# Kernel tuning notes

Hardware: AMD Instinct MI355X
Metric: run time of the kernel (lower is better)

Reference implementation:

```python
import jax, jax.numpy as jnp
import numpy as np

N_NODES = 50000
IN_CH, HID_CH, OUT_CH = 128, 128, 64
N_EDGES = 800000


def setup_inputs() -> dict:
    key = jax.random.key(0)
    k = jax.random.split(key, 6)
    x = jax.random.normal(k[0], (N_NODES, IN_CH), dtype=jnp.float32)
    edge_index = jax.random.randint(k[1], (2, N_EDGES), 0, N_NODES, dtype=jnp.int64)
    # Glorot-ish init for weights
    W1 = jax.random.normal(k[2], (IN_CH, HID_CH), dtype=jnp.float32) * (1.0 / np.sqrt(IN_CH))
    b1 = jnp.zeros((HID_CH,), dtype=jnp.float32)
    W2 = jax.random.normal(k[3], (HID_CH, OUT_CH), dtype=jnp.float32) * (1.0 / np.sqrt(HID_CH))
    b2 = jnp.zeros((OUT_CH,), dtype=jnp.float32)
    return {"x": x, "edge_index": edge_index, "W1": W1, "b1": b1, "W2": W2, "b2": b2}


def _gcn_conv(x, src, dst, W, b, n_nodes):
    """PyG GCNConv: linear, add self-loops, symmetric deg^-1/2 normalization, scatter-add."""
    h = x @ W  # [N, F_out]
    loop = jnp.arange(n_nodes, dtype=src.dtype)
    s = jnp.concatenate([src, loop])  # [E+N]
    d = jnp.concatenate([dst, loop])
    # in-degree on target nodes (including self-loops), edge weight = 1
    deg = jnp.zeros((n_nodes,), dtype=h.dtype).at[d].add(1.0)
    dinv = jnp.where(deg > 0, jax.lax.rsqrt(deg), 0.0)
    norm = dinv[s] * dinv[d]  # [E+N]
    msg = h[s] * norm[:, None]  # [E+N, F_out]
    out = jax.ops.segment_sum(msg, d, num_segments=n_nodes)
    return out + b


def reference(x, edge_index, W1, b1, W2, b2):
    src, dst = edge_index[0], edge_index[1]
    h = _gcn_conv(x, src, dst, W1, b1, N_NODES)
    h = jax.nn.relu(h)
    # dropout in eval mode -> identity
    out = _gcn_conv(h, src, dst, W2, b2, N_NODES)
    return out
```

## Files before the change

kernel.cpp:

```cpp
#include <hip/hip_runtime.h>

typedef __attribute__((ext_vector_type(8))) short bf16x8;
typedef __attribute__((ext_vector_type(4))) float f32x4;

constexpr int NN = 50000;
constexpr int NE = 800000;
constexpr int C1 = 128;
constexpr int C2 = 64;
constexpr int NBK = 196;
constexpr int EPB = 2048;
constexpr int NBLK = (NE + EPB - 1) / EPB;
constexpr int MT = NN / 16;
constexpr int MMB = 250;
constexpr int MMWAVES = MMB * 4;
constexpr int CAP = 8192;

__device__ __forceinline__ unsigned short f2bf(float f) {
    unsigned int u = __float_as_uint(f);
    u += 0x7FFFu + ((u >> 16) & 1u);
    return (unsigned short)(u >> 16);
}
__device__ __forceinline__ float2 bf2f(unsigned int u) {
    return make_float2(__uint_as_float(u << 16), __uint_as_float(u & 0xFFFF0000u));
}
__device__ __forceinline__ bf16x8 pack8(float4 a, float4 b) {
    bf16x8 r;
    r[0] = (short)f2bf(a.x); r[1] = (short)f2bf(a.y);
    r[2] = (short)f2bf(a.z); r[3] = (short)f2bf(a.w);
    r[4] = (short)f2bf(b.x); r[5] = (short)f2bf(b.y);
    r[6] = (short)f2bf(b.z); r[7] = (short)f2bf(b.w);
    return r;
}

__global__ __launch_bounds__(256) void bin_kernel(const int* __restrict__ src,
                                                  const int* __restrict__ dst,
                                                  unsigned int* __restrict__ ebuf,
                                                  int* __restrict__ localOff) {
    __shared__ int lhist[NBK];
    __shared__ int ls[256];
    __shared__ int lcur[NBK];
    __shared__ unsigned int lbuf[EPB];
    const int t = threadIdx.x;
    const int base = blockIdx.x * EPB;
    if (t < NBK) lhist[t] = 0;
    __syncthreads();
    int b[8]; unsigned int p[8];
    #pragma unroll
    for (int i = 0; i < 8; i++) {
        int e = base + i * 256 + t;
        if (e < NE) {
            int s = src[e], d = dst[e];
            b[i] = d >> 8;
            p[i] = ((unsigned int)(d & 255) << 16) | (unsigned int)s;
            atomicAdd(&lhist[b[i]], 1);
        } else b[i] = -1;
    }
    __syncthreads();
    int v = (t < NBK) ? lhist[t] : 0;
    ls[t] = v;
    __syncthreads();
    #pragma unroll
    for (int d = 1; d < 256; d <<= 1) {
        int u = (t >= d) ? ls[t - d] : 0;
        __syncthreads();
        ls[t] += u;
        __syncthreads();
    }
    if (t < NBK) {
        lcur[t] = ls[t] - v;
        localOff[blockIdx.x * 200 + t] = ls[t] - v;
    }
    if (t == NBK - 1) localOff[blockIdx.x * 200 + NBK] = ls[t];
    __syncthreads();
    #pragma unroll
    for (int i = 0; i < 8; i++) {
        if (b[i] >= 0) {
            int lp = atomicAdd(&lcur[b[i]], 1);
            lbuf[lp] = p[i];
        }
    }
    __syncthreads();
    #pragma unroll
    for (int i = 0; i < 8; i++)
        ebuf[base + i * 256 + t] = lbuf[i * 256 + t];
}

__global__ __launch_bounds__(256) void place_kernel(const unsigned int* __restrict__ ebuf,
                                                    const int* __restrict__ localOff,
                                                    unsigned short* __restrict__ esrc,
                                                    int* __restrict__ cnt,
                                                    int* __restrict__ off,
                                                    float* __restrict__ dinv) {
    __shared__ unsigned int lbuf[CAP];
    __shared__ int lhist[256];
    __shared__ int ls[256];
    __shared__ int lcur[256];
    __shared__ int red[256];
    const int t = threadIdx.x;
    const int bkt = blockIdx.x;
    const int node0 = bkt << 8;
    const int nnodes = min(256, NN - node0);

    const int j0 = 2 * t, j1 = 2 * t + 1;
    int s0 = 0, l0 = 0, s1 = 0, l1 = 0;
    if (j0 < NBLK) { s0 = localOff[j0 * 200 + bkt]; l0 = localOff[j0 * 200 + bkt + 1] - s0; }
    if (j1 < NBLK) { s1 = localOff[j1 * 200 + bkt]; l1 = localOff[j1 * 200 + bkt + 1] - s1; }

    red[t] = s0 + s1;
    ls[t] = l0 + l1;
    lhist[t] = 0;
    __syncthreads();
    #pragma unroll
    for (int d = 1; d < 256; d <<= 1) {
        int u = (t >= d) ? ls[t - d] : 0;
        int r = (t + d < 256) ? red[t + d] : 0;
        __syncthreads();
        ls[t] += u;
        red[t] += r;
        __syncthreads();
    }
    const int segBase = red[0];
    const int total = ls[255];
    const int base0 = ls[t] - (l0 + l1);
    const int base1 = base0 + l0;
    const bool fits = (total <= CAP);

    if (fits) {
        const unsigned int* q0 = ebuf + j0 * EPB + s0;
        for (int k = 0; k < l0; k++) lbuf[base0 + k] = q0[k];
        const unsigned int* q1 = ebuf + j1 * EPB + s1;
        for (int k = 0; k < l1; k++) lbuf[base1 + k] = q1[k];
        __syncthreads();
        for (int k = t; k < total; k += 256) atomicAdd(&lhist[lbuf[k] >> 16], 1);
    } else {
        const unsigned int* q0 = ebuf + j0 * EPB + s0;
        for (int k = 0; k < l0; k++) atomicAdd(&lhist[q0[k] >> 16], 1);
        const unsigned int* q1 = ebuf + j1 * EPB + s1;
        for (int k = 0; k < l1; k++) atomicAdd(&lhist[q1[k] >> 16], 1);
    }
    __syncthreads();
    int v = lhist[t];
    ls[t] = v;
    __syncthreads();
    #pragma unroll
    for (int d = 1; d < 256; d <<= 1) {
        int u = (t >= d) ? ls[t - d] : 0;
        __syncthreads();
        ls[t] += u;
        __syncthreads();
    }
    int ex = ls[t] - v;
    lcur[t] = ex;
    if (t < nnodes) {
        cnt[node0 + t] = v;
        off[node0 + t] = segBase + ex;
        dinv[node0 + t] = rsqrtf((float)v + 1.0f);
    }
    __syncthreads();
    if (fits) {
        for (int k = t; k < total; k += 256) {
            unsigned int pp = lbuf[k];
            int lp = atomicAdd(&lcur[pp >> 16], 1);
            esrc[segBase + lp] = (unsigned short)(pp & 0xFFFFu);
        }
    } else {
        const unsigned int* q0 = ebuf + j0 * EPB + s0;
        for (int k = 0; k < l0; k++) {
            unsigned int pp = q0[k];
            int lp = atomicAdd(&lcur[pp >> 16], 1);
            esrc[segBase + lp] = (unsigned short)(pp & 0xFFFFu);
        }
        const unsigned int* q1 = ebuf + j1 * EPB + s1;
        for (int k = 0; k < l1; k++) {
            unsigned int pp = q1[k];
            int lp = atomicAdd(&lcur[pp >> 16], 1);
            esrc[segBase + lp] = (unsigned short)(pp & 0xFFFFu);
        }
    }
}

__global__ __launch_bounds__(256, 2) void mm1_kernel(const float* __restrict__ x,
                                                     const float* __restrict__ W,
                                                     const float* __restrict__ dinv,
                                                     unsigned short* __restrict__ g1s) {
    __shared__ unsigned short wl[4][8][64][8];
    const int t = threadIdx.x;
    for (int i = 0; i < 64; i++) {
        int idx = i * 256 + t;
        int k = idx >> 7, n = idx & 127;
        wl[k >> 5][n >> 4][((k >> 3) & 3) * 16 + (n & 15)][k & 7] = f2bf(W[idx]);
    }
    __syncthreads();
    const int lane = t & 63, lm = lane & 15, quad = lane >> 4;

    bf16x8 bfr[4][8];
    #pragma unroll
    for (int s = 0; s < 4; s++)
        #pragma unroll
        for (int nt = 0; nt < 8; nt++)
            bfr[s][nt] = *(const bf16x8*)&wl[s][nt][lane][0];

    int wg = blockIdx.x * 4 + (t >> 6);
    for (int tile = wg; tile < MT; tile += MMWAVES) {
        int row0 = tile << 4;
        const float* xr = x + (size_t)(row0 + lm) * 128 + quad * 8;
        bf16x8 af[4];
        #pragma unroll
        for (int s = 0; s < 4; s++) {
            float4 p = *(const float4*)(xr + s * 32);
            float4 q = *(const float4*)(xr + s * 32 + 4);
            af[s] = pack8(p, q);
        }
        f32x4 acc[8];
        #pragma unroll
        for (int nt = 0; nt < 8; nt++) acc[nt] = (f32x4){0.f, 0.f, 0.f, 0.f};
        #pragma unroll
        for (int s = 0; s < 4; s++)
            #pragma unroll
            for (int nt = 0; nt < 8; nt++)
                acc[nt] = __builtin_amdgcn_mfma_f32_16x16x32_bf16(af[s], bfr[s][nt],
                                                                  acc[nt], 0, 0, 0);
        float4 dv = *(const float4*)(dinv + row0 + quad * 4);
        float dvv[4] = {dv.x, dv.y, dv.z, dv.w};
        #pragma unroll
        for (int nt = 0; nt < 8; nt++)
            #pragma unroll
            for (int r = 0; r < 4; r++)
                g1s[(size_t)(nt >> 1) * (NN * 32) + (size_t)(row0 + quad * 4 + r) * 32 +
                    (nt & 1) * 16 + lm] = f2bf(acc[nt][r] * dvv[r]);
    }
}

__global__ __launch_bounds__(256, 2) void mm2_kernel(const unsigned short* __restrict__ x2,
                                                     const float* __restrict__ W,
                                                     const float* __restrict__ dinv,
                                                     unsigned short* __restrict__ g2s) {
    __shared__ unsigned short wl[4][4][64][8];
    const int t = threadIdx.x;
    for (int i = 0; i < 32; i++) {
        int idx = i * 256 + t;
        int k = idx >> 6, n = idx & 63;
        wl[k >> 5][n >> 4][((k >> 3) & 3) * 16 + (n & 15)][k & 7] = f2bf(W[idx]);
    }
    __syncthreads();
    const int lane = t & 63, lm = lane & 15, quad = lane >> 4;

    bf16x8 bfr[4][4];
    #pragma unroll
    for (int s = 0; s < 4; s++)
        #pragma unroll
        for (int nt = 0; nt < 4; nt++)
            bfr[s][nt] = *(const bf16x8*)&wl[s][nt][lane][0];

    int wg = blockIdx.x * 4 + (t >> 6);
    for (int tile = wg; tile < MT; tile += MMWAVES) {
        int row0 = tile << 4;
        const bf16x8* xr = (const bf16x8*)(x2 + (size_t)(row0 + lm) * 128 + quad * 8);
        bf16x8 af[4];
        #pragma unroll
        for (int s = 0; s < 4; s++) af[s] = xr[s * 4];
        f32x4 acc[4];
        #pragma unroll
        for (int nt = 0; nt < 4; nt++) acc[nt] = (f32x4){0.f, 0.f, 0.f, 0.f};
        #pragma unroll
        for (int s = 0; s < 4; s++)
            #pragma unroll
            for (int nt = 0; nt < 4; nt++)
                acc[nt] = __builtin_amdgcn_mfma_f32_16x16x32_bf16(af[s], bfr[s][nt],
                                                                  acc[nt], 0, 0, 0);
        float4 dv = *(const float4*)(dinv + row0 + quad * 4);
        float dvv[4] = {dv.x, dv.y, dv.z, dv.w};
        #pragma unroll
        for (int nt = 0; nt < 4; nt++)
            #pragma unroll
            for (int r = 0; r < 4; r++)
                g2s[(size_t)(nt >> 1) * (NN * 32) + (size_t)(row0 + quad * 4 + r) * 32 +
                    (nt & 1) * 16 + lm] = f2bf(acc[nt][r] * dvv[r]);
    }
}

__global__ __launch_bounds__(256) void gp1_kernel(const unsigned int* __restrict__ Gp,
                                                  const unsigned short* __restrict__ esrc,
                                                  const int* __restrict__ off,
                                                  const int* __restrict__ cnt,
                                                  const float* __restrict__ dinv,
                                                  const float* __restrict__ b1,
                                                  unsigned int* __restrict__ x2,
                                                  int pass) {
    const int n = blockIdx.x * 16 + (threadIdx.x >> 4);
    const int p = threadIdx.x & 15;
    float2 a0 = bf2f(Gp[(size_t)n * 16 + p]);
    float2 a1 = make_float2(0.f, 0.f);
    int s0 = off[n], c = cnt[n];
    int i = 0;
    for (; i + 1 < c; i += 2) {
        int sA = esrc[s0 + i];
        int sB = esrc[s0 + i + 1];
        float2 fA = bf2f(Gp[(size_t)sA * 16 + p]);
        float2 fB = bf2f(Gp[(size_t)sB * 16 + p]);
        a0.x += fA.x; a0.y += fA.y;
        a1.x += fB.x; a1.y += fB.y;
    }
    if (i < c) {
        float2 fA = bf2f(Gp[(size_t)esrc[s0 + i] * 16 + p]);
        a0.x += fA.x; a0.y += fA.y;
    }
    a0.x += a1.x; a0.y += a1.y;
    float sc = dinv[n];
    float2 bb = ((const float2*)b1)[pass * 16 + p];
    float lo = fmaxf(sc * a0.x + bb.x, 0.f);
    float hi = fmaxf(sc * a0.y + bb.y, 0.f);
    x2[(size_t)n * 64 + pass * 16 + p] = ((unsigned int)f2bf(hi) << 16) | f2bf(lo);
}

__global__ __launch_bounds__(256) void gp2_kernel(const unsigned int* __restrict__ Gp,
                                                  const unsigned short* __restrict__ esrc,
                                                  const int* __restrict__ off,
                                                  const int* __restrict__ cnt,
                                                  const float* __restrict__ dinv,
                                                  const float* __restrict__ b2,
                                                  float2* __restrict__ out,
                                                  int pass) {
    const int n = blockIdx.x * 16 + (threadIdx.x >> 4);
    const int p = threadIdx.x & 15;
    float2 a0 = bf2f(Gp[(size_t)n * 16 + p]);
    float2 a1 = make_float2(0.f, 0.f);
    int s0 = off[n], c = cnt[n];
    int i = 0;
    for (; i + 1 < c; i += 2) {
        int sA = esrc[s0 + i];
        int sB = esrc[s0 + i + 1];
        float2 fA = bf2f(Gp[(size_t)sA * 16 + p]);
        float2 fB = bf2f(Gp[(size_t)sB * 16 + p]);
        a0.x += fA.x; a0.y += fA.y;
        a1.x += fB.x; a1.y += fB.y;
    }
    if (i < c) {
        float2 fA = bf2f(Gp[(size_t)esrc[s0 + i] * 16 + p]);
        a0.x += fA.x; a0.y += fA.y;
    }
    a0.x += a1.x; a0.y += a1.y;
    float sc = dinv[n];
    float2 bb = ((const float2*)b2)[pass * 16 + p];
    out[(size_t)n * 32 + pass * 16 + p] = make_float2(sc * a0.x + bb.x, sc * a0.y + bb.y);
}

extern "C" void kernel_launch(void* const* d_in, const int* in_sizes, int n_in,
                              void* d_out, int out_size, void* d_ws, size_t ws_size,
                              hipStream_t stream) {
    const float* x  = (const float*)d_in[0];
    const int* edges = (const int*)d_in[1];
    const float* W1 = (const float*)d_in[2];
    const float* b1 = (const float*)d_in[3];
    const float* W2 = (const float*)d_in[4];
    const float* b2 = (const float*)d_in[5];
    const int* src = edges;
    const int* dst = edges + NE;

    int* localOff  = (int*)d_ws;
    unsigned int* ebuf = (unsigned int*)(localOff + 78208);
    unsigned short* esrc = (unsigned short*)(ebuf + (size_t)NBLK * EPB);
    int* cnt       = (int*)(esrc + 800768);
    int* off       = cnt + 50048;
    float* dinv    = (float*)(off + 50048);
    unsigned short* g1s = (unsigned short*)(dinv + 50048);
    unsigned short* x2  = g1s + (size_t)NN * C1;
    unsigned short* g2s = g1s;
    float* out = (float*)d_out;

    bin_kernel<<<NBLK, 256, 0, stream>>>(src, dst, ebuf, localOff);
    place_kernel<<<NBK, 256, 0, stream>>>(ebuf, localOff, esrc, cnt, off, dinv);

    mm1_kernel<<<MMB, 256, 0, stream>>>(x, W1, dinv, g1s);
    for (int pass = 0; pass < 4; pass++)
        gp1_kernel<<<MT, 256, 0, stream>>>((const unsigned int*)g1s + (size_t)pass * NN * 16,
                                           esrc, off, cnt, dinv, b1,
                                           (unsigned int*)x2, pass);

    mm2_kernel<<<MMB, 256, 0, stream>>>(x2, W2, dinv, g2s);
    for (int pass = 0; pass < 2; pass++)
        gp2_kernel<<<MT, 256, 0, stream>>>((const unsigned int*)g2s + (size_t)pass * NN * 16,
                                           esrc, off, cnt, dinv, b2,
                                           (float2*)out, pass);
}
```

Measured before the change: 222.0 us.

## Store projected features row-major and merge per-slice gather passes into single launches

The matmul outputs switch from column-sliced planar buffers (32 bf16 columns per slice) to plain row-major bf16 rows. The multi-pass gather launches are replaced by a single launch per layer, with the column slice taken from the low bits of blockIdx. This cuts launch count, and adjacent blocks now handle all slices of the same nodes at the same time, so edge-index reads are shared in cache. The cost is that each slice pass no longer has a compact 64B-stride table; a gather for one slice touches 64B inside a 256B (or 128B) row, which may lower L2 locality compared with the slice-contiguous layout.

Result: faster. 217.0 us (-2.3%).

```diff
diff --git a/kernel.cpp b/kernel.cpp
--- a/kernel.cpp
+++ b/kernel.cpp
@@ -182,7 +182,7 @@
 __global__ __launch_bounds__(256, 2) void mm1_kernel(const float* __restrict__ x,
                                                      const float* __restrict__ W,
                                                      const float* __restrict__ dinv,
-                                                     unsigned short* __restrict__ g1s) {
+                                                     unsigned short* __restrict__ g1) {
     __shared__ unsigned short wl[4][8][64][8];
     const int t = threadIdx.x;
     for (int i = 0; i < 64; i++) {
@@ -226,15 +226,15 @@
         for (int nt = 0; nt < 8; nt++)
             #pragma unroll
             for (int r = 0; r < 4; r++)
-                g1s[(size_t)(nt >> 1) * (NN * 32) + (size_t)(row0 + quad * 4 + r) * 32 +
-                    (nt & 1) * 16 + lm] = f2bf(acc[nt][r] * dvv[r]);
+                g1[(size_t)(row0 + quad * 4 + r) * 128 + nt * 16 + lm] =
+                    f2bf(acc[nt][r] * dvv[r]);
     }
 }
 
 __global__ __launch_bounds__(256, 2) void mm2_kernel(const unsigned short* __restrict__ x2,
                                                      const float* __restrict__ W,
                                                      const float* __restrict__ dinv,
-                                                     unsigned short* __restrict__ g2s) {
+                                                     unsigned short* __restrict__ g2) {
     __shared__ unsigned short wl[4][4][64][8];
     const int t = threadIdx.x;
     for (int i = 0; i < 32; i++) {
@@ -274,75 +274,77 @@
         for (int nt = 0; nt < 4; nt++)
             #pragma unroll
             for (int r = 0; r < 4; r++)
-                g2s[(size_t)(nt >> 1) * (NN * 32) + (size_t)(row0 + quad * 4 + r) * 32 +
-                    (nt & 1) * 16 + lm] = f2bf(acc[nt][r] * dvv[r]);
-    }
-}
-
-__global__ __launch_bounds__(256) void gp1_kernel(const unsigned int* __restrict__ Gp,
-                                                  const unsigned short* __restrict__ esrc,
-                                                  const int* __restrict__ off,
-                                                  const int* __restrict__ cnt,
-                                                  const float* __restrict__ dinv,
-                                                  const float* __restrict__ b1,
-                                                  unsigned int* __restrict__ x2,
-                                                  int pass) {
-    const int n = blockIdx.x * 16 + (threadIdx.x >> 4);
+                g2[(size_t)(row0 + quad * 4 + r) * 64 + nt * 16 + lm] =
+                    f2bf(acc[nt][r] * dvv[r]);
+    }
+}
+
+__global__ __launch_bounds__(256) void gather1_kernel(const unsigned int* __restrict__ Gp,
+                                                      const unsigned short* __restrict__ esrc,
+                                                      const int* __restrict__ off,
+                                                      const int* __restrict__ cnt,
+                                                      const float* __restrict__ dinv,
+                                                      const float* __restrict__ b1,
+                                                      unsigned int* __restrict__ x2) {
+    const int slice = blockIdx.x & 3;
+    const int n = (blockIdx.x >> 2) * 16 + (threadIdx.x >> 4);
     const int p = threadIdx.x & 15;
-    float2 a0 = bf2f(Gp[(size_t)n * 16 + p]);
+    const int col = slice * 16 + p;
+    float2 a0 = bf2f(Gp[(size_t)n * 64 + col]);
     float2 a1 = make_float2(0.f, 0.f);
     int s0 = off[n], c = cnt[n];
     int i = 0;
     for (; i + 1 < c; i += 2) {
         int sA = esrc[s0 + i];
         int sB = esrc[s0 + i + 1];
-        float2 fA = bf2f(Gp[(size_t)sA * 16 + p]);
-        float2 fB = bf2f(Gp[(size_t)sB * 16 + p]);
+        float2 fA = bf2f(Gp[(size_t)sA * 64 + col]);
+        float2 fB = bf2f(Gp[(size_t)sB * 64 + col]);
         a0.x += fA.x; a0.y += fA.y;
         a1.x += fB.x; a1.y += fB.y;
     }
     if (i < c) {
-        float2 fA = bf2f(Gp[(size_t)esrc[s0 + i] * 16 + p]);
+        float2 fA = bf2f(Gp[(size_t)esrc[s0 + i] * 64 + col]);
         a0.x += fA.x; a0.y += fA.y;
     }
     a0.x += a1.x; a0.y += a1.y;
     float sc = dinv[n];
-    float2 bb = ((const float2*)b1)[pass * 16 + p];
+    float2 bb = ((const float2*)b1)[col];
     float lo = fmaxf(sc * a0.x + bb.x, 0.f);
     float hi = fmaxf(sc * a0.y + bb.y, 0.f);
-    x2[(size_t)n * 64 + pass * 16 + p] = ((unsigned int)f2bf(hi) << 16) | f2bf(lo);
-}
-
-__global__ __launch_bounds__(256) void gp2_kernel(const unsigned int* __restrict__ Gp,
-                                                  const unsigned short* __restrict__ esrc,
-                                                  const int* __restrict__ off,
-                                                  const int* __restrict__ cnt,
-                                                  const float* __restrict__ dinv,
-                                                  const float* __restrict__ b2,
-                                                  float2* __restrict__ out,
-                                                  int pass) {
-    const int n = blockIdx.x * 16 + (threadIdx.x >> 4);
+    x2[(size_t)n * 64 + col] = ((unsigned int)f2bf(hi) << 16) | f2bf(lo);
+}
+
+__global__ __launch_bounds__(256) void gather2_kernel(const unsigned int* __restrict__ Gp,
+                                                      const unsigned short* __restrict__ esrc,
+                                                      const int* __restrict__ off,
+                                                      const int* __restrict__ cnt,
+                                                      const float* __restrict__ dinv,
+                                                      const float* __restrict__ b2,
+                                                      float2* __restrict__ out) {
+    const int slice = blockIdx.x & 1;
+    const int n = (blockIdx.x >> 1) * 16 + (threadIdx.x >> 4);
     const int p = threadIdx.x & 15;
-    float2 a0 = bf2f(Gp[(size_t)n * 16 + p]);
+    const int col = slice * 16 + p;
+    float2 a0 = bf2f(Gp[(size_t)n * 32 + col]);
     float2 a1 = make_float2(0.f, 0.f);
     int s0 = off[n], c = cnt[n];
     int i = 0;
     for (; i + 1 < c; i += 2) {
         int sA = esrc[s0 + i];
         int sB = esrc[s0 + i + 1];
-        float2 fA = bf2f(Gp[(size_t)sA * 16 + p]);
-        float2 fB = bf2f(Gp[(size_t)sB * 16 + p]);
+        float2 fA = bf2f(Gp[(size_t)sA * 32 + col]);
+        float2 fB = bf2f(Gp[(size_t)sB * 32 + col]);
         a0.x += fA.x; a0.y += fA.y;
         a1.x += fB.x; a1.y += fB.y;
     }
     if (i < c) {
-        float2 fA = bf2f(Gp[(size_t)esrc[s0 + i] * 16 + p]);
+        float2 fA = bf2f(Gp[(size_t)esrc[s0 + i] * 32 + col]);
         a0.x += fA.x; a0.y += fA.y;
     }
     a0.x += a1.x; a0.y += a1.y;
     float sc = dinv[n];
-    float2 bb = ((const float2*)b2)[pass * 16 + p];
-    out[(size_t)n * 32 + pass * 16 + p] = make_float2(sc * a0.x + bb.x, sc * a0.y + bb.y);
+    float2 bb = ((const float2*)b2)[col];
+    out[(size_t)n * 32 + col] = make_float2(sc * a0.x + bb.x, sc * a0.y + bb.y);
 }
 
 extern "C" void kernel_launch(void* const* d_in, const int* in_sizes, int n_in,
@@ -363,23 +365,19 @@
     int* cnt       = (int*)(esrc + 800768);
     int* off       = cnt + 50048;
     float* dinv    = (float*)(off + 50048);
-    unsigned short* g1s = (unsigned short*)(dinv + 50048);
-    unsigned short* x2  = g1s + (size_t)NN * C1;
-    unsigned short* g2s = g1s;
+    unsigned short* g1 = (unsigned short*)(dinv + 50048);
+    unsigned short* x2 = g1 + (size_t)NN * C1;
+    unsigned short* g2 = g1;
     float* out = (float*)d_out;
 
     bin_kernel<<<NBLK, 256, 0, stream>>>(src, dst, ebuf, localOff);
     place_kernel<<<NBK, 256, 0, stream>>>(ebuf, localOff, esrc, cnt, off, dinv);
 
-    mm1_kernel<<<MMB, 256, 0, stream>>>(x, W1, dinv, g1s);
-    for (int pass = 0; pass < 4; pass++)
-        gp1_kernel<<<MT, 256, 0, stream>>>((const unsigned int*)g1s + (size_t)pass * NN * 16,
-                                           esrc, off, cnt, dinv, b1,
-                                           (unsigned int*)x2, pass);
-
-    mm2_kernel<<<MMB, 256, 0, stream>>>(x2, W2, dinv, g2s);
-    for (int pass = 0; pass < 2; pass++)
-        gp2_kernel<<<MT, 256, 0, stream>>>((const unsigned int*)g2s + (size_t)pass * NN * 16,
-                                           esrc, off, cnt, dinv, b2,
-                                           (float2*)out, pass);
-}
+    mm1_kernel<<<MMB, 256, 0, stream>>>(x, W1, dinv, g1);
+    gather1_kernel<<<MT * 4, 256, 0, stream>>>((const unsigned int*)g1, esrc, off, cnt,
+                                               dinv, b1, (unsigned int*)x2);
+
+    mm2_kernel<<<MMB, 256, 0, stream>>>(x2, W2, dinv, g2);
+    gather2_kernel<<<MT * 2, 256, 0, stream>>>((const unsigned int*)g2, esrc, off, cnt,
+                                               dinv, b2, (float2*)out);
+}
```
